# Optimization experiments

Hardware: AMD Instinct MI355X
Metric: run time of the kernel (lower is better)

## Reference

```python
import jax, jax.numpy as jnp
import numpy as np

HIDDEN = 51
INPUT = 1
OUTPUT = 1
BATCH = 4096
SEQ = 999


def setup_inputs() -> dict:
    key = jax.random.key(0)
    ks = jax.random.split(key, 7)
    s = 1.0 / np.sqrt(HIDDEN)  # PyTorch default LSTM/Linear init scale
    u = lambda k, shape: jax.random.uniform(k, shape, jnp.float32, -s, s)
    return {
        "input": jax.random.normal(ks[0], (BATCH, SEQ, INPUT), jnp.float32),
        "W_ih": u(ks[1], (4 * HIDDEN, INPUT)),
        "W_hh": u(ks[2], (4 * HIDDEN, HIDDEN)),
        "b_ih": u(ks[3], (4 * HIDDEN,)),
        "b_hh": u(ks[4], (4 * HIDDEN,)),
        "W_fc": u(ks[5], (OUTPUT, HIDDEN)),
        "b_fc": u(ks[6], (OUTPUT,)),
        "future": 0,
    }


def reference(input, W_ih, W_hh, b_ih, b_hh, W_fc, b_fc, future):
    # Single-layer LSTM (PyTorch gate order i, f, g, o) scanned over time,
    # followed by a per-timestep Linear -> (batch, seq+future, output).
    def step(carry, x_t):
        h, c = carry
        gates = x_t @ W_ih.T + b_ih + h @ W_hh.T + b_hh  # (B, 4H)
        i, f, g, o = jnp.split(gates, 4, axis=-1)
        c = jax.nn.sigmoid(f) * c + jax.nn.sigmoid(i) * jnp.tanh(g)
        h = jax.nn.sigmoid(o) * jnp.tanh(c)
        return (h, c), h

    B = input.shape[0]
    h0 = jnp.zeros((B, HIDDEN), input.dtype)
    c0 = jnp.zeros((B, HIDDEN), input.dtype)
    xs = jnp.swapaxes(input, 0, 1)  # (T, B, I)
    (h, c), hs = jax.lax.scan(step, (h0, c0), xs)
    ys = hs @ W_fc.T + b_fc  # (T, B, O)

    # static Python int, so a trace-time loop is fine).
    y = ys[-1]
    extra = []
    for _ in range(future):
        (h, c), hn = step((h, c), y)
        y = hn @ W_fc.T + b_fc
        extra.append(y)
    if extra:
        ys = jnp.concatenate([ys, jnp.stack(extra, 0)], axis=0)
    return jnp.swapaxes(ys, 0, 1)  # (B, T+future, O)
```

## Files before the change

### kernel.cpp

```cpp
#include <hip/hip_runtime.h>
#include <hip/hip_bf16.h>

#define HID   51
#define MR    208
#define SEQT  999
#define CH    111
#define NCH   9
#define EPB   16
#define XST   17
#define NTH   512
#define BSTR  72

typedef __attribute__((ext_vector_type(8))) short  short8;
typedef __attribute__((ext_vector_type(4))) float  floatx4;

__global__ void prep_kernel(const float* __restrict__ W_hh,
                            const float* __restrict__ W_ih,
                            const float* __restrict__ W_fc,
                            __hip_bfloat16* __restrict__ A_ext)
{
    const float K1 = 1.442695040889f;
    int idx = blockIdx.x * blockDim.x + threadIdx.x;
    if (idx >= MR * 64) return;
    int r = idx >> 6, k = idx & 63;
    int u = r >> 2, gate = r & 3;
    float v = 0.f;
    if (r == 204) {
        if (k < HID) v = W_fc[k];
    } else if (u < HID) {
        float s = (gate == 2) ? (-2.f * K1) : (-K1);
        if (k < HID)      v = s * W_hh[(gate * HID + u) * HID + k];
        else if (k == 51) v = s * W_ih[gate * HID + u];
    }
    A_ext[idx] = __float2bfloat16(v);
}

__launch_bounds__(NTH)
__global__ void lstm_mfma_kernel(const float* __restrict__ x,
                                 const float* __restrict__ b_ih,
                                 const float* __restrict__ b_hh,
                                 const float* __restrict__ b_fc,
                                 const __hip_bfloat16* __restrict__ A_ext,
                                 float* __restrict__ out)
{
    __shared__ __hip_bfloat16 bcol[2][16 * BSTR];
    __shared__ float x_lds[(CH + 1) * XST];
    __shared__ float y_lds[CH * XST];

    const int tid  = threadIdx.x;
    const int w    = tid >> 6;
    const int lane = tid & 63;
    const int e    = lane & 15;
    const int g4   = lane >> 4;
    const int e0   = blockIdx.x * EPB;

    const int  nt = (w < 5) ? 2 : 1;
    const int  T0 = (w < 5) ? 2 * w : (w + 5);
    const bool w7 = (w == 7);
    const bool yln = w7 && (g4 == 3);
    const bool xsv = w7 && (g4 == 0);

    const float K1  = 1.442695040889f;
    const float K2N = -2.885390081777f;

    short8  A0[2], A1[2];
    floatx4 bq[2];
    float   cs[2];
    int     uu[2], wrow[2];

#pragma unroll
    for (int i = 0; i < 2; ++i) {
        A0[i] = short8{0,0,0,0,0,0,0,0}; A1[i] = A0[i];
        bq[i] = floatx4{0.f,0.f,0.f,0.f}; cs[i] = 0.f; uu[i] = 63; wrow[i] = 63;
    }
#pragma unroll
    for (int i = 0; i < 2; ++i) {
        if (i < nt) {
            int T = T0 + i;
            int m = T * 16 + e;
            int u = 4 * T + g4;
            A0[i] = *(const short8*)&A_ext[m * 64 + g4 * 8];
            A1[i] = *(const short8*)&A_ext[m * 64 + 32 + g4 * 8];
            uu[i] = u;
            wrow[i] = (u < HID) ? u : 63;
            if (u < HID) {
#pragma unroll
                for (int gg = 0; gg < 4; ++gg) {
                    float s = (gg == 2) ? (-2.f * K1) : (-K1);
                    bq[i][gg] = s * (b_ih[gg * HID + u] + b_hh[gg * HID + u]);
                }
            }
        }
    }

    for (int i = tid; i < 16 * BSTR; i += NTH) {
        bcol[0][i] = __float2bfloat16(0.f);
        bcol[1][i] = __float2bfloat16(0.f);
    }
    __syncthreads();
    if (tid < EPB)
        bcol[0][tid * BSTR + 51] = __float2bfloat16(x[(size_t)(e0 + tid) * SEQT]);
    const float bfc = b_fc[0];

    __syncthreads();

    for (int tc = 0; tc < NCH; ++tc) {
        const int t0 = tc * CH;
        for (int i2 = tid; i2 < (CH + 1) * EPB; i2 += NTH) {
            int ee = i2 / (CH + 1), tt = i2 % (CH + 1);
            int t = t0 + tt;
            x_lds[tt * XST + ee] = (t < SEQT) ? x[(size_t)(e0 + ee) * SEQT + t] : 0.f;
        }
        __syncthreads();

        for (int tt = 0; tt < CH; ++tt) {
            const int t  = t0 + tt;
            const int rp = t & 1, wp = rp ^ 1;

            short8 B0 = *(const short8*)&bcol[rp][e * BSTR + g4 * 8];
            short8 B1 = *(const short8*)&bcol[rp][e * BSTR + 32 + g4 * 8];
            const floatx4 z = {0.f, 0.f, 0.f, 0.f};

            floatx4 p0 = __builtin_amdgcn_mfma_f32_16x16x32_bf16(A0[0], B0, bq[0], 0, 0, 0);
            floatx4 q0 = __builtin_amdgcn_mfma_f32_16x16x32_bf16(A1[0], B1, z,     0, 0, 0);
            floatx4 p1, q1;
            if (nt == 2) {
                p1 = __builtin_amdgcn_mfma_f32_16x16x32_bf16(A0[1], B0, bq[1], 0, 0, 0);
                q1 = __builtin_amdgcn_mfma_f32_16x16x32_bf16(A1[1], B1, z,     0, 0, 0);
            }

#pragma unroll
            for (int i = 0; i < 2; ++i) {
                if (i < nt) {
                    floatx4 acc = (i == 0) ? (p0 + q0) : (p1 + q1);

                    float Ei = __builtin_amdgcn_exp2f(acc[0]);
                    float Ef = __builtin_amdgcn_exp2f(acc[1]);
                    float Eg = __builtin_amdgcn_exp2f(acc[2]);
                    float Eo = __builtin_amdgcn_exp2f(acc[3]);
                    float sf   = __builtin_amdgcn_rcpf(1.f + Ef);
                    float Rig  = __builtin_amdgcn_rcpf(fmaf(Ei, Eg, (Ei + Eg) + 1.f));
                    float tK   = fmaf(-K2N, Eg, K2N);
                    cs[i] = fmaf(sf, cs[i], tK * Rig);
                    float Ec  = __builtin_amdgcn_exp2f(cs[i]);
                    float Roc = __builtin_amdgcn_rcpf(fmaf(Eo, Ec, (Eo + Ec) + 1.f));
                    float h   = (1.f - Ec) * Roc;

                    bcol[wp][e * BSTR + wrow[i]] =
                        __float2bfloat16((uu[i] < HID) ? h : 0.f);
                    if (i == 0 && yln) y_lds[tt * XST + e] = acc[0] + bfc;
                }
            }
            if (xsv) bcol[wp][e * BSTR + 51] =
                         __float2bfloat16(x_lds[(tt + 1) * XST + e]);

            __syncthreads();
        }
        __syncthreads();

        for (int i2 = tid; i2 < CH * EPB; i2 += NTH) {
            int ee = i2 / CH, tt = i2 % CH;
            int t = t0 + tt - 1;
            if (t >= 0)
                out[(size_t)(e0 + ee) * SEQT + t] = y_lds[tt * XST + ee];
        }
        __syncthreads();
    }

    if (w7) {
        short8 B0 = *(const short8*)&bcol[1][e * BSTR + g4 * 8];
        short8 B1 = *(const short8*)&bcol[1][e * BSTR + 32 + g4 * 8];
        const floatx4 z = {0.f, 0.f, 0.f, 0.f};
        floatx4 p = __builtin_amdgcn_mfma_f32_16x16x32_bf16(A0[0], B0, bq[0], 0, 0, 0);
        floatx4 q = __builtin_amdgcn_mfma_f32_16x16x32_bf16(A1[0], B1, z,     0, 0, 0);
        floatx4 acc = p + q;
        if (g4 == 3)
            out[(size_t)(e0 + e) * SEQT + (SEQT - 1)] = acc[0] + bfc;
    }
}

extern "C" void kernel_launch(void* const* d_in, const int* in_sizes, int n_in,
                              void* d_out, int out_size, void* d_ws, size_t ws_size,
                              hipStream_t stream) {
    const float* x    = (const float*)d_in[0];
    const float* W_ih = (const float*)d_in[1];
    const float* W_hh = (const float*)d_in[2];
    const float* b_ih = (const float*)d_in[3];
    const float* b_hh = (const float*)d_in[4];
    const float* W_fc = (const float*)d_in[5];
    const float* b_fc = (const float*)d_in[6];
    float* out = (float*)d_out;

    __hip_bfloat16* A_ext = (__hip_bfloat16*)d_ws;

    prep_kernel<<<(MR * 64 + 255) / 256, 256, 0, stream>>>(W_hh, W_ih, W_fc, A_ext);
    lstm_mfma_kernel<<<4096 / EPB, NTH, 0, stream>>>(x, b_ih, b_hh,
                                                     b_fc, A_ext, out);
}
```

Measured before the change: 528.2 us.

## Use 7 waves per block with uneven tile assignment and chained MFMA accumulation

```diff
diff --git a/kernel.cpp b/kernel.cpp
--- a/kernel.cpp
+++ b/kernel.cpp
@@ -8,7 +8,7 @@
 #define NCH   9
 #define EPB   16
 #define XST   17
-#define NTH   512
+#define NTH   448
 #define BSTR  72
 
 typedef __attribute__((ext_vector_type(8))) short  short8;
@@ -54,34 +54,35 @@
     const int g4   = lane >> 4;
     const int e0   = blockIdx.x * EPB;
 
-    const int  nt = (w < 5) ? 2 : 1;
-    const int  T0 = (w < 5) ? 2 * w : (w + 5);
-    const bool w7 = (w == 7);
-    const bool yln = w7 && (g4 == 3);
-    const bool xsv = w7 && (g4 == 0);
+    const int starts[7] = {0, 2, 4, 6, 9, 11, 10};
+    const int cnts[7]   = {2, 2, 2, 3, 1, 2, 1};
+    const int  tstart = starts[w];
+    const int  tcnt   = cnts[w];
+    const bool yw  = (w == 5);
+    const bool yln = yw && (g4 == 3);
+    const bool xsv = (w == 6) && (g4 == 0);
 
     const float K1  = 1.442695040889f;
     const float K2N = -2.885390081777f;
 
-    short8  A0[2], A1[2];
-    floatx4 bq[2];
-    float   cs[2];
-    int     uu[2], wrow[2];
+    short8  A0[3], A1[3];
+    floatx4 bq[3];
+    float   cs[3];
+    int     wrow[3];
 
 #pragma unroll
-    for (int i = 0; i < 2; ++i) {
+    for (int i = 0; i < 3; ++i) {
         A0[i] = short8{0,0,0,0,0,0,0,0}; A1[i] = A0[i];
-        bq[i] = floatx4{0.f,0.f,0.f,0.f}; cs[i] = 0.f; uu[i] = 63; wrow[i] = 63;
+        bq[i] = floatx4{0.f,0.f,0.f,0.f}; cs[i] = 0.f; wrow[i] = 63;
     }
 #pragma unroll
-    for (int i = 0; i < 2; ++i) {
-        if (i < nt) {
-            int T = T0 + i;
+    for (int i = 0; i < 3; ++i) {
+        if (i < tcnt) {
+            int T = tstart + i;
             int m = T * 16 + e;
             int u = 4 * T + g4;
             A0[i] = *(const short8*)&A_ext[m * 64 + g4 * 8];
             A1[i] = *(const short8*)&A_ext[m * 64 + 32 + g4 * 8];
-            uu[i] = u;
             wrow[i] = (u < HID) ? u : 63;
             if (u < HID) {
 #pragma unroll
@@ -119,20 +120,12 @@
 
             short8 B0 = *(const short8*)&bcol[rp][e * BSTR + g4 * 8];
             short8 B1 = *(const short8*)&bcol[rp][e * BSTR + 32 + g4 * 8];
-            const floatx4 z = {0.f, 0.f, 0.f, 0.f};
-
-            floatx4 p0 = __builtin_amdgcn_mfma_f32_16x16x32_bf16(A0[0], B0, bq[0], 0, 0, 0);
-            floatx4 q0 = __builtin_amdgcn_mfma_f32_16x16x32_bf16(A1[0], B1, z,     0, 0, 0);
-            floatx4 p1, q1;
-            if (nt == 2) {
-                p1 = __builtin_amdgcn_mfma_f32_16x16x32_bf16(A0[1], B0, bq[1], 0, 0, 0);
-                q1 = __builtin_amdgcn_mfma_f32_16x16x32_bf16(A1[1], B1, z,     0, 0, 0);
-            }
 
 #pragma unroll
-            for (int i = 0; i < 2; ++i) {
-                if (i < nt) {
-                    floatx4 acc = (i == 0) ? (p0 + q0) : (p1 + q1);
+            for (int i = 0; i < 3; ++i) {
+                if (i < tcnt) {
+                    floatx4 acc = __builtin_amdgcn_mfma_f32_16x16x32_bf16(A0[i], B0, bq[i], 0, 0, 0);
+                    acc = __builtin_amdgcn_mfma_f32_16x16x32_bf16(A1[i], B1, acc, 0, 0, 0);
 
                     float Ei = __builtin_amdgcn_exp2f(acc[0]);
                     float Ef = __builtin_amdgcn_exp2f(acc[1]);
@@ -146,9 +139,8 @@
                     float Roc = __builtin_amdgcn_rcpf(fmaf(Eo, Ec, (Eo + Ec) + 1.f));
                     float h   = (1.f - Ec) * Roc;
 
-                    bcol[wp][e * BSTR + wrow[i]] =
-                        __float2bfloat16((uu[i] < HID) ? h : 0.f);
-                    if (i == 0 && yln) y_lds[tt * XST + e] = acc[0] + bfc;
+                    bcol[wp][e * BSTR + wrow[i]] = __float2bfloat16(h);
+                    if (i == 1 && yln) y_lds[tt * XST + e] = acc[0] + bfc;
                 }
             }
             if (xsv) bcol[wp][e * BSTR + 51] =
@@ -167,13 +159,11 @@
         __syncthreads();
     }
 
-    if (w7) {
+    if (yw) {
         short8 B0 = *(const short8*)&bcol[1][e * BSTR + g4 * 8];
         short8 B1 = *(const short8*)&bcol[1][e * BSTR + 32 + g4 * 8];
-        const floatx4 z = {0.f, 0.f, 0.f, 0.f};
-        floatx4 p = __builtin_amdgcn_mfma_f32_16x16x32_bf16(A0[0], B0, bq[0], 0, 0, 0);
-        floatx4 q = __builtin_amdgcn_mfma_f32_16x16x32_bf16(A1[0], B1, z,     0, 0, 0);
-        floatx4 acc = p + q;
+        floatx4 acc = __builtin_amdgcn_mfma_f32_16x16x32_bf16(A0[1], B0, bq[1], 0, 0, 0);
+        acc = __builtin_amdgcn_mfma_f32_16x16x32_bf16(A1[1], B1, acc, 0, 0, 0);
         if (g4 == 3)
             out[(size_t)(e0 + e) * SEQT + (SEQT - 1)] = acc[0] + bfc;
     }
```

Result: faster. 505.2 us (-4.4%).
